# Performance work log

Hardware: AMD Instinct MI355X
Metric: run time of the kernel (lower is better)

## Reference

```python
import jax, jax.numpy as jnp
import numpy as np

B, S, DIN, DQ, DK = 4, 2048, 1024, 64, 64
NEG_INF = -jnp.inf


def _make_mask(sq, sk):
    # Mirrors createMask: causal mask (-inf where key_idx > query_idx),
    # except 3 randomly chosen (row, col) 'global token' pairs left at 0.
    # torch version uses random.sample; we use a fixed numpy RNG for determinism.
    rng = np.random.default_rng(0)
    g_rows = rng.choice(sk, 3, replace=False)  # sampled from range(lrlen)
    g_cols = rng.choice(sq, 3, replace=False)  # sampled from range(sequence_len)
    row = jnp.arange(sq)[:, None]
    col = jnp.arange(sk)[None, :]
    mask = jnp.where(col > row, NEG_INF, 0.0).astype(jnp.float32)
    mask = mask.at[jnp.asarray(g_rows), jnp.asarray(g_cols)].set(0.0)
    return mask  # [sq, sk]


def setup_inputs() -> dict:
    key = jax.random.key(0)
    ks = jax.random.split(key, 9)
    sc = 1.0 / np.sqrt(DIN)
    return {
        "q": jax.random.normal(ks[0], (B, S, DIN), jnp.float32),
        "k": jax.random.normal(ks[1], (B, S, DIN), jnp.float32),
        "v": jax.random.normal(ks[2], (B, S, DIN), jnp.float32),
        "Wq": jax.random.normal(ks[3], (DIN, DQ), jnp.float32) * sc,
        "bq": jax.random.normal(ks[4], (DQ,), jnp.float32) * sc,
        "Wk": jax.random.normal(ks[5], (DIN, DK), jnp.float32) * sc,
        "bk": jax.random.normal(ks[6], (DK,), jnp.float32) * sc,
        "Wv": jax.random.normal(ks[7], (DIN, DK), jnp.float32) * sc,
        "bv": jax.random.normal(ks[8], (DK,), jnp.float32) * sc,
    }


def reference(q, k, v, Wq, bq, Wk, bk, Wv, bv):
    Q = q @ Wq + bq            # [B,S,DQ]
    K = k @ Wk + bk            # [B,S,DK]
    V = v @ Wv + bv            # [B,S,DK]
    scores = jnp.einsum("bqd,bkd->bqk", Q, K)  # [B,S,S]
    mask = _make_mask(scores.shape[-2], scores.shape[-1])
    denom = jnp.asarray(K.shape[-1], jnp.float32) ** 0.5
    # NOTE: original adds mask BEFORE dividing by sqrt(d_k); -inf survives division.
    attn = jax.nn.softmax((scores + mask) / denom, axis=-1)
    return jnp.einsum("bqk,bkd->bqd", attn, V)  # [B,S,DK]
```

## Files before the change

### kernel.cpp

```cpp
#include <hip/hip_runtime.h>
#include <cstdint>
#include <cstddef>
#include <math.h>

#define SEQ    2048
#define NBATCH 4
#define DIN    1024
#define DH     64

typedef __attribute__((ext_vector_type(8))) short  short8;
typedef __attribute__((ext_vector_type(4))) float  floatx4;
typedef __attribute__((ext_vector_type(4))) unsigned short ushort4v;

#define MFMA16(a, b, c) __builtin_amdgcn_mfma_f32_16x16x32_bf16((a), (b), (c), 0, 0, 0)

__device__ __forceinline__ unsigned short f2bf(float x) {
  unsigned u = __float_as_uint(x);
  return (unsigned short)((u + 0x8000u) >> 16);
}
__device__ __forceinline__ float bf2f(unsigned short h) {
  return __uint_as_float(((unsigned)h) << 16);
}

__device__ __forceinline__ void async_cp4(const void* g, void* l) {
  __builtin_amdgcn_global_load_lds(
      (const __attribute__((address_space(1))) void*)g,
      (__attribute__((address_space(3))) void*)l, 4, 0, 0);
}
__device__ __forceinline__ void async_cp16(const void* g, void* l) {
  __builtin_amdgcn_global_load_lds(
      (const __attribute__((address_space(1))) void*)g,
      (__attribute__((address_space(3))) void*)l, 16, 0, 0);
}

namespace nprng {

struct PCG64 {
  __uint128_t state, inc;
  bool has_uint32;
  uint32_t uinteger;
};

static inline void pcg_step(PCG64 &g) {
  const __uint128_t MULT =
      (((__uint128_t)0x2360ed051fc65da4ULL) << 64) | 0x4385df649fccf645ULL;
  g.state = g.state * MULT + g.inc;
}

static inline uint64_t pcg_output(const PCG64 &g) {
  uint64_t hi = (uint64_t)(g.state >> 64);
  uint64_t lo = (uint64_t)g.state;
  uint64_t x = hi ^ lo;
  unsigned rot = (unsigned)(g.state >> 122) & 63u;
  return (x >> rot) | (x << ((64u - rot) & 63u));
}

static inline uint64_t pcg_next64(PCG64 &g) { pcg_step(g); return pcg_output(g); }

static inline uint32_t pcg_next32(PCG64 &g) {
  if (g.has_uint32) { g.has_uint32 = false; return g.uinteger; }
  uint64_t n = pcg_next64(g);
  g.has_uint32 = true;
  g.uinteger = (uint32_t)(n >> 32);
  return (uint32_t)(n & 0xffffffffu);
}

static inline void pcg_seed_from_seedseq0(PCG64 &g) {
  const uint32_t MULT_A = 0x931e8875u;
  const uint32_t MULT_B = 0x58f38dedu;
  const uint32_t MIX_L  = 0xca01f9ddu;
  const uint32_t MIX_R  = 0x4973f715u;
  uint32_t hc = 0x43b0d7e5u;
  uint32_t pool[4];
  for (int i = 0; i < 4; i++) {
    uint32_t v = 0u;
    v ^= hc; hc *= MULT_A; v *= hc; v ^= v >> 16;
    pool[i] = v;
  }
  for (int is = 0; is < 4; is++) {
    for (int id = 0; id < 4; id++) {
      if (is == id) continue;
      uint32_t h = pool[is];
      h ^= hc; hc *= MULT_A; h *= hc; h ^= h >> 16;
      uint32_t r = (pool[id] * MIX_L) ^ (h * MIX_R);
      r ^= r >> 16;
      pool[id] = r;
    }
  }
  uint32_t hb = 0x8b51f9ddu;
  uint32_t w[8];
  for (int i = 0; i < 8; i++) {
    uint32_t v = pool[i & 3];
    v ^= hb; hb *= MULT_B; v *= hb; v ^= v >> 16;
    w[i] = v;
  }
  uint64_t sv[4];
  for (int k = 0; k < 4; k++)
    sv[k] = (uint64_t)w[2 * k] | ((uint64_t)w[2 * k + 1] << 32);
  __uint128_t initstate = (((__uint128_t)sv[0]) << 64) | sv[1];
  __uint128_t initseq   = (((__uint128_t)sv[2]) << 64) | sv[3];
  g.state = 0; g.inc = (initseq << 1) | 1;
  pcg_step(g);
  g.state += initstate;
  pcg_step(g);
  g.has_uint32 = false; g.uinteger = 0;
}

static inline uint32_t bounded32(PCG64 &g, uint32_t rng ) {
  if (rng == 0) return 0;
  const uint32_t rng_excl = rng + 1u;
  uint64_t m = (uint64_t)pcg_next32(g) * (uint64_t)rng_excl;
  uint32_t leftover = (uint32_t)m;
  if (leftover < rng_excl) {
    const uint32_t threshold = (uint32_t)(0xffffffffu - rng) % rng_excl;
    while (leftover < threshold) {
      m = (uint64_t)pcg_next32(g) * (uint64_t)rng_excl;
      leftover = (uint32_t)m;
    }
  }
  return (uint32_t)(m >> 32);
}

static inline void choice3_2048(PCG64 &g, long long idx[3]) {
  const int pop = 2048, sz = 3;
  uint64_t hs[4] = { (uint64_t)-1, (uint64_t)-1, (uint64_t)-1, (uint64_t)-1 };
  const uint64_t mask = 3;
  for (int j = pop - sz; j < pop; j++) {
    uint64_t val = (uint64_t)bounded32(g, (uint32_t)j);
    uint64_t loc = val & mask;
    while (hs[loc] != (uint64_t)-1 && hs[loc] != val) loc = (loc + 1) & mask;
    if (hs[loc] == (uint64_t)-1) {
      hs[loc] = val;
      idx[j - pop + sz] = (long long)val;
    } else {
      loc = (uint64_t)j & mask;
      while (hs[loc] != (uint64_t)-1) loc = (loc + 1) & mask;
      hs[loc] = (uint64_t)j;
      idx[j - pop + sz] = (long long)j;
    }
  }
  for (int i = 2; i >= 1; i--) {
    uint32_t j = bounded32(g, (uint32_t)i);
    long long t = idx[j]; idx[j] = idx[i]; idx[i] = t;
  }
}

}

__global__ __launch_bounds__(256) void wtrans_kernel(
    const float* __restrict__ Wq, const float* __restrict__ Wk,
    const float* __restrict__ Wv, unsigned short* __restrict__ WTc) {
  int idx = blockIdx.x * 256 + threadIdx.x;
  int p   = idx >> 16;
  int rem = idx & 65535;
  int n   = rem >> 10;
  int k   = rem & 1023;
  const float* W = (p == 0) ? Wq : (p == 1) ? Wk : Wv;
  unsigned short v = f2bf(W[k * 64 + n]);
  int dst = ((p * 8 + (k >> 7)) * 64 + n) * 128 + (k & 127);
  WTc[dst] = v;
}

__global__ __launch_bounds__(256, 3) void proj_kernel(
    const float* __restrict__ xq, const float* __restrict__ xk,
    const float* __restrict__ xv, const unsigned short* __restrict__ WTc,
    const float* __restrict__ bq, const float* __restrict__ bk,
    const float* __restrict__ bv,
    unsigned short* __restrict__ QP, unsigned short* __restrict__ KP,
    unsigned short* __restrict__ VPT) {
  const int m0g  = blockIdx.x * 32;
  const int proj = m0g >> 13;
  const int m0   = m0g & 8191;
  const float* X    = (proj == 0) ? xq : (proj == 1) ? xk : xv;
  const float* bias = (proj == 0) ? bq : (proj == 1) ? bk : bv;

  const int tid  = threadIdx.x;
  const int w    = tid >> 6;
  const int l    = tid & 63;
  const int quad = l >> 4;
  const int lx   = l & 15;
  const int mr   = (w & 1) * 16;
  const int nc   = (w >> 1) * 32;

  __shared__ float          Xs[32 * 132];
  __shared__ unsigned short Ws[16 * 520];
  __shared__ float          Cs[32][68];

  const float* Xblk = X + (size_t)m0 * DIN;
  const unsigned short* Wpj = WTc + (size_t)proj * 8 * 8192;

  floatx4 acc0 = {0.f, 0.f, 0.f, 0.f}, acc1 = acc0;

  for (int kc = 0; kc < 8; kc++) {
#pragma unroll
    for (int i = 0; i < 8; i++) {
      const int r = 8 * w + i;
      const float* g = Xblk + (size_t)r * DIN + kc * 128;
      async_cp4(g + l,      &Xs[r * 132]);
      async_cp4(g + 64 + l, &Xs[r * 132 + 64]);
    }
#pragma unroll
    for (int i = 0; i < 4; i++) {
      const int g4 = 4 * w + i;
      const unsigned short* gsrc = Wpj + (size_t)kc * 8192 + g4 * 512;
      async_cp16((const char*)gsrc + l * 16, &Ws[g4 * 520]);
    }
    __syncthreads();

#pragma unroll
    for (int ks = 0; ks < 4; ks++) {
      const float* ap = &Xs[(mr + lx) * 132 + ks * 32 + quad * 8];
      const float4 f0 = *(const float4*)ap;
      const float4 f1 = *(const float4*)(ap + 4);
      short8 a;
      a[0] = f2bf(f0.x); a[1] = f2bf(f0.y); a[2] = f2bf(f0.z); a[3] = f2bf(f0.w);
      a[4] = f2bf(f1.x); a[5] = f2bf(f1.y); a[6] = f2bf(f1.z); a[7] = f2bf(f1.w);
      const int c0 = nc + lx, c1 = nc + 16 + lx;
      const short8 b0 = *(const short8*)&Ws[(c0 >> 2) * 520 + (c0 & 3) * 128 + ks * 32 + quad * 8];
      const short8 b1 = *(const short8*)&Ws[(c1 >> 2) * 520 + (c1 & 3) * 128 + ks * 32 + quad * 8];
      acc0 = MFMA16(a, b0, acc0);
      acc1 = MFMA16(a, b1, acc1);
    }
    __syncthreads();
  }

  const float bb0 = bias[nc + lx], bb1 = bias[nc + 16 + lx];
#pragma unroll
  for (int i = 0; i < 4; i++) {
    Cs[mr + quad * 4 + i][nc + lx]      = acc0[i] + bb0;
    Cs[mr + quad * 4 + i][nc + 16 + lx] = acc1[i] + bb1;
  }
  __syncthreads();

  if (proj < 2) {
    unsigned short* outp = (proj == 0) ? QP : KP;
    const int row = tid >> 3;
    const int d0  = (tid & 7) * 8;
    short8 v;
#pragma unroll
    for (int j = 0; j < 8; j++) v[j] = (short)f2bf(Cs[row][d0 + j]);
    *(short8*)(outp + (size_t)(m0 + row) * 64 + d0) = v;
  } else {
    const int dim = tid >> 2;
    const int s0  = (tid & 3) * 8;
    const int bq_ = m0 >> 11;
    const int sq  = (m0 & 2047) + s0;
    short8 v;
#pragma unroll
    for (int j = 0; j < 8; j++) v[j] = (short)f2bf(Cs[s0 + j][dim]);
    *(short8*)(VPT + ((size_t)bq_ * 64 + dim) * SEQ + sq) = v;
  }
}

__global__ __launch_bounds__(256, 2) void attn_kernel(
    const unsigned short* __restrict__ QP, const unsigned short* __restrict__ KP,
    const unsigned short* __restrict__ VPT, float* __restrict__ out,
    int R0, int C0, int R1, int C1, int R2, int C2) {
  const int b    = blockIdx.y;
  const int bx   = blockIdx.x;
  const int qi   = (bx & 1) ? (127 - (bx >> 1)) : (bx >> 1);
  const int q0   = qi * 16;
  const int tid  = threadIdx.x;
  const int w    = tid >> 6;
  const int l    = tid & 63;
  const int quad = l >> 4;
  const int lx   = l & 15;

  __shared__ unsigned short Ps[4][16][72];
  __shared__ float Os[4][16][64];
  __shared__ float mS[4][16], lS[4][16];
  __shared__ float lgS[3];
  __shared__ int   lgF[3];

  const unsigned short* Qb = QP + ((size_t)b * SEQ + q0) * 64;
  const unsigned short* Kb = KP + (size_t)b * SEQ * 64;
  const unsigned short* Vb = VPT + (size_t)b * 64 * SEQ;

  const short8 aq0 = *(const short8*)(Qb + (size_t)lx * 64 + quad * 8);
  const short8 aq1 = *(const short8*)(Qb + (size_t)lx * 64 + 32 + quad * 8);

  floatx4 O[4];
  float m_i[4], l_i[4];
#pragma unroll
  for (int c = 0; c < 4; c++) O[c] = (floatx4){0.f, 0.f, 0.f, 0.f};
#pragma unroll
  for (int i = 0; i < 4; i++) { m_i[i] = -INFINITY; l_i[i] = 0.f; }

  const int T = (q0 + 79) >> 6;

  for (int t = w; t < T; t += 4) {
    const int k0 = t << 6;
    const bool mT = (t == T - 1);

    short8 kf[8], vf[8];
#pragma unroll
    for (int c = 0; c < 4; c++) {
#pragma unroll
      for (int s = 0; s < 2; s++) {
        kf[c * 2 + s] = *(const short8*)(Kb + (size_t)(k0 + 16 * c + lx) * 64 + s * 32 + quad * 8);
        vf[s * 4 + c] = *(const short8*)(Vb + (size_t)(16 * c + lx) * SEQ + k0 + s * 32 + quad * 8);
      }
    }

    floatx4 sc[4];
#pragma unroll
    for (int c = 0; c < 4; c++) {
      sc[c] = (floatx4){0.f, 0.f, 0.f, 0.f};
      sc[c] = MFMA16(aq0, kf[2 * c], sc[c]);
      sc[c] = MFMA16(aq1, kf[2 * c + 1], sc[c]);
    }

    float mt[4], al[4];
#pragma unroll
    for (int i = 0; i < 4; i++) {
      const int rowg = q0 + quad * 4 + i;
      float vmax = -INFINITY;
#pragma unroll
      for (int c = 0; c < 4; c++) {
        float v = sc[c][i] * 0.125f;
        if (mT && (k0 + 16 * c + lx) > rowg) v = -INFINITY;
        sc[c][i] = v;
        vmax = fmaxf(vmax, v);
      }
      mt[i] = vmax;
    }
#pragma unroll
    for (int i = 0; i < 4; i++) {
#pragma unroll
      for (int off = 8; off >= 1; off >>= 1)
        mt[i] = fmaxf(mt[i], __shfl_xor(mt[i], off));
      const float mn = fmaxf(m_i[i], mt[i]);
      al[i] = __expf(m_i[i] - mn);
      m_i[i] = mn;
      float s = 0.f;
#pragma unroll
      for (int c = 0; c < 4; c++) {
        float p = __expf(sc[c][i] - mn);
        Ps[w][quad * 4 + i][16 * c + lx] = f2bf(p);
        s += p;
      }
#pragma unroll
      for (int off = 8; off >= 1; off >>= 1) s += __shfl_xor(s, off);
      l_i[i] = l_i[i] * al[i] + s;
    }
#pragma unroll
    for (int c = 0; c < 4; c++)
#pragma unroll
      for (int i = 0; i < 4; i++) O[c][i] *= al[i];
    asm volatile("" ::: "memory");
    const short8 pf0 = *(const short8*)&Ps[w][lx][quad * 8];
    const short8 pf1 = *(const short8*)&Ps[w][lx][32 + quad * 8];
#pragma unroll
    for (int c = 0; c < 4; c++) {
      O[c] = MFMA16(pf0, vf[c],     O[c]);
      O[c] = MFMA16(pf1, vf[4 + c], O[c]);
    }
  }

  if (lx == 0) {
#pragma unroll
    for (int i = 0; i < 4; i++) {
      mS[w][quad * 4 + i] = m_i[i];
      lS[w][quad * 4 + i] = l_i[i];
    }
  }
#pragma unroll
  for (int c = 0; c < 4; c++)
#pragma unroll
    for (int i = 0; i < 4; i++) Os[w][quad * 4 + i][16 * c + lx] = O[c][i];

  if (w == 0) {
#pragma unroll
    for (int p = 0; p < 3; p++) {
      const int R = (p == 0) ? R0 : (p == 1) ? R1 : R2;
      const int C = (p == 0) ? C0 : (p == 1) ? C1 : C2;
      const int act = (R >= q0 && R < q0 + 16 && C > R);
      float d = 0.f;
      if (act) {
        const float qv = bf2f(QP[((size_t)b * SEQ + R) * 64 + l]);
        const float kv = bf2f(KP[((size_t)b * SEQ + C) * 64 + l]);
        d = qv * kv;
#pragma unroll
        for (int off = 32; off >= 1; off >>= 1) d += __shfl_xor(d, off);
        d *= 0.125f;
      }
      if (l == 0) { lgF[p] = act; lgS[p] = d; }
    }
  }
  __syncthreads();

  {
    const int row = tid >> 4;
    const int d0  = (tid & 15) * 4;
    const int Rs[3] = {R0, R1, R2};
    const int Cs3[3] = {C0, C1, C2};

    float mf = -INFINITY;
#pragma unroll
    for (int w4 = 0; w4 < 4; w4++) mf = fmaxf(mf, mS[w4][row]);
#pragma unroll
    for (int p = 0; p < 3; p++)
      if (lgF[p] && (Rs[p] - q0) == row) mf = fmaxf(mf, lgS[p]);

    float lf = 0.f;
    float o0 = 0.f, o1 = 0.f, o2 = 0.f, o3 = 0.f;
#pragma unroll
    for (int w4 = 0; w4 < 4; w4++) {
      const float a = __expf(mS[w4][row] - mf);
      lf += a * lS[w4][row];
      const float* op = &Os[w4][row][d0];
      o0 += a * op[0]; o1 += a * op[1]; o2 += a * op[2]; o3 += a * op[3];
    }
#pragma unroll
    for (int p = 0; p < 3; p++) {
      if (lgF[p] && (Rs[p] - q0) == row) {
        const float pe = __expf(lgS[p] - mf);
        lf += pe;
        const int C = Cs3[p];
        o0 += pe * bf2f(Vb[(size_t)(d0 + 0) * SEQ + C]);
        o1 += pe * bf2f(Vb[(size_t)(d0 + 1) * SEQ + C]);
        o2 += pe * bf2f(Vb[(size_t)(d0 + 2) * SEQ + C]);
        o3 += pe * bf2f(Vb[(size_t)(d0 + 3) * SEQ + C]);
      }
    }
    const float inv = 1.0f / lf;
    float4 r;
    r.x = o0 * inv; r.y = o1 * inv; r.z = o2 * inv; r.w = o3 * inv;
    *(float4*)(out + ((size_t)b * SEQ + q0 + row) * 64 + d0) = r;
  }
}

extern "C" void kernel_launch(void* const* d_in, const int* in_sizes, int n_in,
                              void* d_out, int out_size, void* d_ws,
                              size_t ws_size, hipStream_t stream) {
  const float* xq = (const float*)d_in[0];
  const float* xk = (const float*)d_in[1];
  const float* xv = (const float*)d_in[2];
  const float* Wq = (const float*)d_in[3];
  const float* bq = (const float*)d_in[4];
  const float* Wk = (const float*)d_in[5];
  const float* bk = (const float*)d_in[6];
  const float* Wv = (const float*)d_in[7];
  const float* bv = (const float*)d_in[8];
  float* out = (float*)d_out;

  unsigned short* QP  = (unsigned short*)d_ws;
  unsigned short* KP  = QP + (size_t)NBATCH * SEQ * 64;
  unsigned short* VPT = KP + (size_t)NBATCH * SEQ * 64;
  unsigned short* WTc = VPT + (size_t)NBATCH * 64 * SEQ;

  nprng::PCG64 g;
  nprng::pcg_seed_from_seedseq0(g);
  long long rows[3], cols[3];
  nprng::choice3_2048(g, rows);
  nprng::choice3_2048(g, cols);

  wtrans_kernel<<<768, 256, 0, stream>>>(Wq, Wk, Wv, WTc);

  proj_kernel<<<768, 256, 0, stream>>>(xq, xk, xv, WTc, bq, bk, bv, QP, KP, VPT);

  dim3 agrid(SEQ / 16, NBATCH);
  attn_kernel<<<agrid, 256, 0, stream>>>(
      QP, KP, VPT, out, (int)rows[0], (int)cols[0], (int)rows[1], (int)cols[1],
      (int)rows[2], (int)cols[2]);
}
```

Before: 168.7 us.

## Store Q/K/V in MFMA fragment order and double-buffer projection LDS stages

The projection kernel now writes Q, K and V directly in the per-lane MFMA fragment layout. Each attention wave can then load its K/V tiles with fully contiguous 16-byte-per-lane reads instead of strided row and column gathers. The projection K-loop is also double-buffered in LDS so the next chunk's async copies overlap the current chunk's MFMAs, dropping one barrier per iteration. LDS use roughly doubles and the occupancy hint drops from 3 to 2 blocks, and the global-token scalar lookups need more complex address arithmetic.

```diff
diff --git a/kernel.cpp b/kernel.cpp
--- a/kernel.cpp
+++ b/kernel.cpp
@@ -161,13 +161,13 @@
   WTc[dst] = v;
 }
 
-__global__ __launch_bounds__(256, 3) void proj_kernel(
+__global__ __launch_bounds__(256, 2) void proj_kernel(
     const float* __restrict__ xq, const float* __restrict__ xk,
     const float* __restrict__ xv, const unsigned short* __restrict__ WTc,
     const float* __restrict__ bq, const float* __restrict__ bk,
     const float* __restrict__ bv,
-    unsigned short* __restrict__ QP, unsigned short* __restrict__ KP,
-    unsigned short* __restrict__ VPT) {
+    unsigned short* __restrict__ Qf, unsigned short* __restrict__ Kf,
+    unsigned short* __restrict__ Vf) {
   const int m0g  = blockIdx.x * 32;
   const int proj = m0g >> 13;
   const int m0   = m0g & 8191;
@@ -182,16 +182,16 @@
   const int mr   = (w & 1) * 16;
   const int nc   = (w >> 1) * 32;
 
-  __shared__ float          Xs[32 * 132];
-  __shared__ unsigned short Ws[16 * 520];
-  __shared__ float          Cs[32][68];
+  __shared__ __align__(16) char LDSbuf[2 * 16896 + 2 * 16640];
 
   const float* Xblk = X + (size_t)m0 * DIN;
   const unsigned short* Wpj = WTc + (size_t)proj * 8 * 8192;
 
   floatx4 acc0 = {0.f, 0.f, 0.f, 0.f}, acc1 = acc0;
 
-  for (int kc = 0; kc < 8; kc++) {
+  auto stage = [&](int kc, int buf) {
+    float* Xs = (float*)(LDSbuf + buf * 16896);
+    unsigned short* Ws = (unsigned short*)(LDSbuf + 2 * 16896 + buf * 16640);
 #pragma unroll
     for (int i = 0; i < 8; i++) {
       const int r = 8 * w + i;
@@ -205,8 +205,15 @@
       const unsigned short* gsrc = Wpj + (size_t)kc * 8192 + g4 * 512;
       async_cp16((const char*)gsrc + l * 16, &Ws[g4 * 520]);
     }
+  };
+
+  stage(0, 0);
+  for (int kc = 0; kc < 8; kc++) {
     __syncthreads();
-
+    if (kc < 7) stage(kc + 1, (kc + 1) & 1);
+    const float* Xs = (const float*)(LDSbuf + (kc & 1) * 16896);
+    const unsigned short* Ws =
+        (const unsigned short*)(LDSbuf + 2 * 16896 + (kc & 1) * 16640);
 #pragma unroll
     for (int ks = 0; ks < 4; ks++) {
       const float* ap = &Xs[(mr + lx) * 132 + ks * 32 + quad * 8];
@@ -221,9 +228,10 @@
       acc0 = MFMA16(a, b0, acc0);
       acc1 = MFMA16(a, b1, acc1);
     }
-    __syncthreads();
-  }
-
+  }
+  __syncthreads();
+
+  float (*Cs)[68] = (float(*)[68])LDSbuf;
   const float bb0 = bias[nc + lx], bb1 = bias[nc + 16 + lx];
 #pragma unroll
   for (int i = 0; i < 4; i++) {
@@ -232,29 +240,40 @@
   }
   __syncthreads();
 
-  if (proj < 2) {
-    unsigned short* outp = (proj == 0) ? QP : KP;
-    const int row = tid >> 3;
-    const int d0  = (tid & 7) * 8;
+  const int bq_ = m0 >> 11;
+  const int s0  = m0 & 2047;
+  if (proj == 0) {
+    const int ti = tid >> 7, s = (tid >> 6) & 1, ll = tid & 63;
+    const int lxx = ll & 15, qq = ll >> 4;
     short8 v;
 #pragma unroll
-    for (int j = 0; j < 8; j++) v[j] = (short)f2bf(Cs[row][d0 + j]);
-    *(short8*)(outp + (size_t)(m0 + row) * 64 + d0) = v;
+    for (int j = 0; j < 8; j++) v[j] = (short)f2bf(Cs[ti * 16 + lxx][s * 32 + qq * 8 + j]);
+    char* dst = (char*)Qf + ((size_t)(bq_ * 128 + (s0 >> 4) + ti)) * 2048 + s * 1024 + ll * 16;
+    *(short8*)dst = v;
+  } else if (proj == 1) {
+    const int ci = tid >> 7, s = (tid >> 6) & 1, ll = tid & 63;
+    const int lxx = ll & 15, qq = ll >> 4;
+    const int c = ((s0 >> 4) & 3) + ci;
+    short8 v;
+#pragma unroll
+    for (int j = 0; j < 8; j++) v[j] = (short)f2bf(Cs[ci * 16 + lxx][s * 32 + qq * 8 + j]);
+    char* dst = (char*)Kf + ((size_t)(bq_ * 32 + (s0 >> 6))) * 8192 + (c * 2 + s) * 1024 + ll * 16;
+    *(short8*)dst = v;
   } else {
-    const int dim = tid >> 2;
-    const int s0  = (tid & 3) * 8;
-    const int bq_ = m0 >> 11;
-    const int sq  = (m0 & 2047) + s0;
+    const int c = tid >> 6, ll = tid & 63;
+    const int lxx = ll & 15, qq = ll >> 4;
+    const int sh = (s0 >> 5) & 1;
     short8 v;
 #pragma unroll
-    for (int j = 0; j < 8; j++) v[j] = (short)f2bf(Cs[s0 + j][dim]);
-    *(short8*)(VPT + ((size_t)bq_ * 64 + dim) * SEQ + sq) = v;
+    for (int j = 0; j < 8; j++) v[j] = (short)f2bf(Cs[qq * 8 + j][c * 16 + lxx]);
+    char* dst = (char*)Vf + ((size_t)(bq_ * 32 + (s0 >> 6))) * 8192 + (sh * 4 + c) * 1024 + ll * 16;
+    *(short8*)dst = v;
   }
 }
 
 __global__ __launch_bounds__(256, 2) void attn_kernel(
-    const unsigned short* __restrict__ QP, const unsigned short* __restrict__ KP,
-    const unsigned short* __restrict__ VPT, float* __restrict__ out,
+    const unsigned short* __restrict__ Qf, const unsigned short* __restrict__ Kf,
+    const unsigned short* __restrict__ Vf, float* __restrict__ out,
     int R0, int C0, int R1, int C1, int R2, int C2) {
   const int b    = blockIdx.y;
   const int bx   = blockIdx.x;
@@ -272,12 +291,9 @@
   __shared__ float lgS[3];
   __shared__ int   lgF[3];
 
-  const unsigned short* Qb = QP + ((size_t)b * SEQ + q0) * 64;
-  const unsigned short* Kb = KP + (size_t)b * SEQ * 64;
-  const unsigned short* Vb = VPT + (size_t)b * 64 * SEQ;
-
-  const short8 aq0 = *(const short8*)(Qb + (size_t)lx * 64 + quad * 8);
-  const short8 aq1 = *(const short8*)(Qb + (size_t)lx * 64 + 32 + quad * 8);
+  const char* Qc = (const char*)Qf + ((size_t)(b * 128 + qi)) * 2048 + l * 16;
+  const short8 aq0 = *(const short8*)Qc;
+  const short8 aq1 = *(const short8*)(Qc + 1024);
 
   floatx4 O[4];
   float m_i[4], l_i[4];
@@ -292,14 +308,13 @@
     const int k0 = t << 6;
     const bool mT = (t == T - 1);
 
+    const char* Kc = (const char*)Kf + ((size_t)(b * 32 + t)) * 8192 + l * 16;
+    const char* Vc = (const char*)Vf + ((size_t)(b * 32 + t)) * 8192 + l * 16;
     short8 kf[8], vf[8];
 #pragma unroll
-    for (int c = 0; c < 4; c++) {
-#pragma unroll
-      for (int s = 0; s < 2; s++) {
-        kf[c * 2 + s] = *(const short8*)(Kb + (size_t)(k0 + 16 * c + lx) * 64 + s * 32 + quad * 8);
-        vf[s * 4 + c] = *(const short8*)(Vb + (size_t)(16 * c + lx) * SEQ + k0 + s * 32 + quad * 8);
-      }
+    for (int f = 0; f < 8; f++) {
+      kf[f] = *(const short8*)(Kc + f * 1024);
+      vf[f] = *(const short8*)(Vc + f * 1024);
     }
 
     floatx4 sc[4];
@@ -377,9 +392,13 @@
       const int act = (R >= q0 && R < q0 + 16 && C > R);
       float d = 0.f;
       if (act) {
-        const float qv = bf2f(QP[((size_t)b * SEQ + R) * 64 + l]);
-        const float kv = bf2f(KP[((size_t)b * SEQ + C) * 64 + l]);
-        d = qv * kv;
+        const int dd = l;
+        const char* qa = (const char*)Qf + ((size_t)(b * 128 + (R >> 4))) * 2048 +
+                         (dd >> 5) * 1024 + ((R & 15) + ((dd >> 3) & 3) * 16) * 16 + (dd & 7) * 2;
+        const char* ka = (const char*)Kf + ((size_t)(b * 32 + (C >> 6))) * 8192 +
+                         (((C >> 4) & 3) * 2 + (dd >> 5)) * 1024 +
+                         ((C & 15) + ((dd >> 3) & 3) * 16) * 16 + (dd & 7) * 2;
+        d = bf2f(*(const unsigned short*)qa) * bf2f(*(const unsigned short*)ka);
 #pragma unroll
         for (int off = 32; off >= 1; off >>= 1) d += __shfl_xor(d, off);
         d *= 0.125f;
@@ -417,10 +436,16 @@
         const float pe = __expf(lgS[p] - mf);
         lf += pe;
         const int C = Cs3[p];
-        o0 += pe * bf2f(Vb[(size_t)(d0 + 0) * SEQ + C]);
-        o1 += pe * bf2f(Vb[(size_t)(d0 + 1) * SEQ + C]);
-        o2 += pe * bf2f(Vb[(size_t)(d0 + 2) * SEQ + C]);
-        o3 += pe * bf2f(Vb[(size_t)(d0 + 3) * SEQ + C]);
+        float vv[4];
+#pragma unroll
+        for (int j = 0; j < 4; j++) {
+          const int dim = d0 + j;
+          const char* va = (const char*)Vf + ((size_t)(b * 32 + (C >> 6))) * 8192 +
+                           (((C >> 5) & 1) * 4 + (dim >> 4)) * 1024 +
+                           ((dim & 15) + ((C >> 3) & 3) * 16) * 16 + (C & 7) * 2;
+          vv[j] = bf2f(*(const unsigned short*)va);
+        }
+        o0 += pe * vv[0]; o1 += pe * vv[1]; o2 += pe * vv[2]; o3 += pe * vv[3];
       }
     }
     const float inv = 1.0f / lf;
@@ -444,10 +469,10 @@
   const float* bv = (const float*)d_in[8];
   float* out = (float*)d_out;
 
-  unsigned short* QP  = (unsigned short*)d_ws;
-  unsigned short* KP  = QP + (size_t)NBATCH * SEQ * 64;
-  unsigned short* VPT = KP + (size_t)NBATCH * SEQ * 64;
-  unsigned short* WTc = VPT + (size_t)NBATCH * 64 * SEQ;
+  unsigned short* Qf  = (unsigned short*)d_ws;
+  unsigned short* Kf  = Qf + (size_t)NBATCH * SEQ * 64;
+  unsigned short* Vf  = Kf + (size_t)NBATCH * SEQ * 64;
+  unsigned short* WTc = Vf + (size_t)NBATCH * SEQ * 64;
 
   nprng::PCG64 g;
   nprng::pcg_seed_from_seedseq0(g);
@@ -457,10 +482,10 @@
 
   wtrans_kernel<<<768, 256, 0, stream>>>(Wq, Wk, Wv, WTc);
 
-  proj_kernel<<<768, 256, 0, stream>>>(xq, xk, xv, WTc, bq, bk, bv, QP, KP, VPT);
+  proj_kernel<<<768, 256, 0, stream>>>(xq, xk, xv, WTc, bq, bk, bv, Qf, Kf, Vf);
 
   dim3 agrid(SEQ / 16, NBATCH);
   attn_kernel<<<agrid, 256, 0, stream>>>(
-      QP, KP, VPT, out, (int)rows[0], (int)cols[0], (int)rows[1], (int)cols[1],
+      Qf, Kf, Vf, out, (int)rows[0], (int)cols[0], (int)rows[1], (int)cols[1],
       (int)rows[2], (int)cols[2]);
 }
```

Measured after the change: 158.4 us. 1.06x faster.
